# Optimization experiments

Measured on AMD Instinct MI355X. Metric: run time of the kernel, lower is better.

Reference implementation:

```python
import jax, jax.numpy as jnp
import numpy as np

N = 50000      # nodes
E = 800000     # edges
F_IN = 11      # node feature dim (from docstring)
HID = 128      # hidden_channels
NC = 16        # num_classes
G = 64         # number of graphs in the batch
NEG_SLOPE = 0.2


def gat_layer(h_in, src, dst, W, a_src, a_dst, b, n_nodes):
    """Single-head GATConv with self-loops (PyG defaults, edge_attr unused)."""
    h = h_in @ W                                   # [N, C]
    alpha_s = h @ a_src                            # [N]
    alpha_d = h @ a_dst                            # [N]
    e = jax.nn.leaky_relu(alpha_s[src] + alpha_d[dst], NEG_SLOPE)  # [E']
    # segment softmax over incoming edges of each dst node
    m = jax.ops.segment_max(e, dst, num_segments=n_nodes)
    ex = jnp.exp(e - m[dst])
    den = jax.ops.segment_sum(ex, dst, num_segments=n_nodes)
    alpha = ex / den[dst]                          # [E']
    out = jax.ops.segment_sum(alpha[:, None] * h[src], dst, num_segments=n_nodes)
    return out + b


def setup_inputs() -> dict:
    key = jax.random.key(0)
    ks = jax.random.split(key, 16)
    glorot = lambda k, fi, fo: jax.random.normal(k, (fi, fo), jnp.float32) * np.float32(1.0 / np.sqrt(fi))
    inp = {
        "x": jax.random.normal(ks[0], (N, F_IN), jnp.float32),
        "edge_index": jax.random.randint(ks[1], (2, E), 0, N, dtype=jnp.int32),
        "edge_attr": jax.random.normal(ks[2], (E, 17), jnp.float32),
        "batch": jnp.sort(jax.random.randint(ks[3], (N,), 0, G, dtype=jnp.int32)),
        "W1": glorot(ks[4], F_IN, HID), "as1": jax.random.normal(ks[5], (HID,)) * 0.1,
        "ad1": jax.random.normal(ks[6], (HID,)) * 0.1, "b1": jnp.zeros((HID,), jnp.float32),
        "W2": glorot(ks[7], HID, HID), "as2": jax.random.normal(ks[8], (HID,)) * 0.1,
        "ad2": jax.random.normal(ks[9], (HID,)) * 0.1, "b2": jnp.zeros((HID,), jnp.float32),
        "W3": glorot(ks[10], HID, NC), "as3": jax.random.normal(ks[11], (NC,)) * 0.1,
        "ad3": jax.random.normal(ks[12], (NC,)) * 0.1, "b3": jnp.zeros((NC,), jnp.float32),
    }
    return inp


def reference(x, edge_index, edge_attr, batch,
              W1, as1, ad1, b1, W2, as2, ad2, b2, W3, as3, ad3, b3):
    n = x.shape[0]
    loop = jnp.arange(n, dtype=edge_index.dtype)
    src = jnp.concatenate([edge_index[0], loop])   # add self-loops
    dst = jnp.concatenate([edge_index[1], loop])

    h = jax.nn.relu(gat_layer(x, src, dst, W1, as1, ad1, b1, n))
    h = jax.nn.relu(gat_layer(h, src, dst, W2, as2, ad2, b2, n))
    h = jax.nn.relu(gat_layer(h, src, dst, W3, as3, ad3, b3, n))

    # global mean pool over graphs
    sums = jax.ops.segment_sum(h, batch, num_segments=G)              # [G, NC]
    cnts = jax.ops.segment_sum(jnp.ones((n,), h.dtype), batch, num_segments=G)
    pooled = sums / jnp.maximum(cnts, 1.0)[:, None]
    # dropout is identity in eval mode
    return jax.nn.sigmoid(pooled)
```

## Files before the change

kernel.cpp:

```cpp
#include <hip/hip_runtime.h>
#include <hip/hip_bf16.h>
#include <hip/hip_fp16.h>
#include <math.h>

#define N_NODES 50000
#define N_EDGES 800000
#define F_IN    11
#define HID     128
#define NC      16
#define NG      64
#define E_TOT   (N_EDGES + N_NODES)
#define NBLK_POOL ((N_NODES + 255) / 256)
#define NEG_SLOPE 0.2f

#define NB   ((N_NODES + 63) >> 6)
#define BCAP 4096

typedef _Float16 half_t;
typedef __attribute__((ext_vector_type(4))) _Float16 half4;
typedef __attribute__((ext_vector_type(8))) _Float16 half8;
typedef __attribute__((ext_vector_type(4))) float f32x4;

__device__ __forceinline__ float leaky(float x) { return x >= 0.f ? x : NEG_SLOPE * x; }


__global__ void zero_nb_kernel(int* __restrict__ gcount) {
    int i = threadIdx.x;
    if (i < NB) gcount[i] = 0;
}

__global__ __launch_bounds__(256) void bucket_hist_kernel(const int* __restrict__ ei,
                                                          int* __restrict__ gcount) {
    __shared__ int cnt[NB];
    int tid = threadIdx.x;
    for (int i = tid; i < NB; i += 256) cnt[i] = 0;
    __syncthreads();
    int e0 = blockIdx.x * 4096 + tid;
#pragma unroll
    for (int k = 0; k < 16; ++k) {
        int e = e0 + k * 256;
        if (e < N_EDGES) atomicAdd(&cnt[ei[N_EDGES + e] >> 6], 1);
    }
    __syncthreads();
    for (int i = tid; i < NB; i += 256)
        if (cnt[i]) atomicAdd(&gcount[i], cnt[i]);
}

__global__ void scanB_kernel(const int* __restrict__ gcount, int* __restrict__ bOff,
                             int* __restrict__ gcur) {
    __shared__ int ls[1024];
    int tid = threadIdx.x;
    int v = 0;
    if (tid < NB) {
        int sl = N_NODES - (tid << 6);
        sl = sl > 64 ? 64 : sl;
        v = gcount[tid] + sl;
    }
    ls[tid] = v;
    __syncthreads();
    for (int ofs = 1; ofs < 1024; ofs <<= 1) {
        int x = (tid >= ofs) ? ls[tid - ofs] : 0;
        __syncthreads();
        ls[tid] += x;
        __syncthreads();
    }
    int excl = (tid > 0) ? ls[tid - 1] : 0;
    if (tid < NB) { bOff[tid] = excl; gcur[tid] = excl; }
    if (tid == 0) bOff[NB] = E_TOT;
}

__global__ __launch_bounds__(256) void bucket_scatter_kernel(const int* __restrict__ ei,
                                                             int* __restrict__ gcur,
                                                             uint2* __restrict__ pairs) {
    __shared__ int cnt[NB];
    __shared__ int base[NB];
    int tid = threadIdx.x;
    for (int i = tid; i < NB; i += 256) cnt[i] = 0;
    __syncthreads();
    int s[16], d[16];
    int e0 = blockIdx.x * 4096 + tid;
#pragma unroll
    for (int k = 0; k < 16; ++k) {
        int e = e0 + k * 256;
        if (e < N_EDGES) { s[k] = ei[e]; d[k] = ei[N_EDGES + e]; }
        else if (e < E_TOT) { s[k] = d[k] = e - N_EDGES; }
        else d[k] = -1;
        if (d[k] >= 0) atomicAdd(&cnt[d[k] >> 6], 1);
    }
    __syncthreads();
    for (int i = tid; i < NB; i += 256)
        base[i] = cnt[i] ? atomicAdd(&gcur[i], cnt[i]) : 0;
    __syncthreads();
    for (int i = tid; i < NB; i += 256) cnt[i] = 0;
    __syncthreads();
#pragma unroll
    for (int k = 0; k < 16; ++k) {
        if (d[k] >= 0) {
            int b = d[k] >> 6;
            int r = atomicAdd(&cnt[b], 1);
            pairs[base[b] + r] = make_uint2((unsigned)s[k], (unsigned)d[k]);
        }
    }
}

__global__ __launch_bounds__(256) void csr_finalize_kernel(const uint2* __restrict__ pairs,
                                                           const int* __restrict__ bOff,
                                                           int* __restrict__ off,
                                                           int* __restrict__ csr) {
    __shared__ uint2 lp[BCAP];
    __shared__ int deg[64], offs[65], cnt[64];
    int b = blockIdx.x, tid = threadIdx.x;
    int d0 = b << 6;
    int nd = N_NODES - d0; nd = nd > 64 ? 64 : nd;
    int lo = bOff[b], hi = bOff[b + 1], n = hi - lo;
    if (tid < 64) { deg[tid] = 0; cnt[tid] = 0; }
    __syncthreads();
    bool staged = (n <= BCAP);
    for (int i = tid; i < n; i += 256) {
        uint2 p = pairs[lo + i];
        if (staged) lp[i] = p;
        atomicAdd(&deg[(int)p.y - d0], 1);
    }
    __syncthreads();
    if (tid == 0) {
        int a = 0;
#pragma unroll
        for (int i = 0; i < 64; ++i) { offs[i] = a; a += deg[i]; }
        offs[64] = a;
    }
    __syncthreads();
    if (tid < nd) off[d0 + tid] = lo + offs[tid];
    if (b == (int)gridDim.x - 1 && tid == 0) off[N_NODES] = E_TOT;
    for (int i = tid; i < n; i += 256) {
        uint2 p = staged ? lp[i] : pairs[lo + i];
        int ld = (int)p.y - d0;
        int r = atomicAdd(&cnt[ld], 1);
        csr[lo + offs[ld] + r] = (int)p.x;
    }
}


__global__ void prep_w2t_kernel(const float* __restrict__ W2, half_t* __restrict__ W2T) {
    int id = blockIdx.x * 256 + threadIdx.x;
    if (id < HID * HID) {
        int col = id >> 7, k = id & 127;
        W2T[id] = (half_t)W2[k * HID + col];
    }
}


__global__ void gemm1_kernel(const float* __restrict__ x, const float* __restrict__ W,
                             const float* __restrict__ a_s, const float* __restrict__ a_d,
                             half_t* __restrict__ h16,
                             float* __restrict__ asv, float* __restrict__ adv) {
    __shared__ float xr[F_IN];
    __shared__ float red[4];
    int row = blockIdx.x;
    int t = threadIdx.x;
    if (t < F_IN) xr[t] = x[row * F_IN + t];
    __syncthreads();
    float acc = 0.f;
#pragma unroll
    for (int k = 0; k < F_IN; ++k) acc = fmaf(xr[k], W[k * HID + t], acc);
    h16[(size_t)row * HID + t] = (half_t)acc;
    float ps = acc * a_s[t], pd = acc * a_d[t];
#pragma unroll
    for (int m = 32; m; m >>= 1) { ps += __shfl_xor(ps, m); pd += __shfl_xor(pd, m); }
    int lane = t & 63, wid = t >> 6;
    if (lane == 0) { red[wid * 2] = ps; red[wid * 2 + 1] = pd; }
    __syncthreads();
    if (t == 0) { asv[row] = red[0] + red[2]; adv[row] = red[1] + red[3]; }
}


__global__ __launch_bounds__(256) void gemm2_mfma_kernel(
    const half_t* __restrict__ A, const half_t* __restrict__ W2T,
    const float* __restrict__ a_s, const float* __restrict__ a_d,
    half_t* __restrict__ outp, float* __restrict__ asv, float* __restrict__ adv) {
    int wid = threadIdx.x >> 6;
    int lane = threadIdx.x & 63;
    int row0 = blockIdx.x * 64 + wid * 16;
    int rl = lane & 15;
    int kg = lane >> 4;
    int arow = row0 + rl;
    if (arow >= N_NODES) arow = N_NODES - 1;
    const half8* Ap = (const half8*)(A + (size_t)arow * HID);
    half8 afrag[4];
#pragma unroll
    for (int kk = 0; kk < 4; ++kk) afrag[kk] = Ap[kk * 4 + kg];
    float ps[4] = {0.f, 0.f, 0.f, 0.f}, pd[4] = {0.f, 0.f, 0.f, 0.f};
#pragma unroll
    for (int ct = 0; ct < 8; ++ct) {
        f32x4 acc = {0.f, 0.f, 0.f, 0.f};
        const half8* Bp = (const half8*)(W2T + (size_t)(ct * 16 + rl) * HID);
#pragma unroll
        for (int kk = 0; kk < 4; ++kk)
            acc = __builtin_amdgcn_mfma_f32_16x16x32_f16(afrag[kk], Bp[kk * 4 + kg], acc, 0, 0, 0);
        int col = ct * 16 + rl;
        float as_c = a_s[col], ad_c = a_d[col];
#pragma unroll
        for (int i = 0; i < 4; ++i) {
            int r = row0 + kg * 4 + i;
            ps[i] = fmaf(acc[i], as_c, ps[i]);
            pd[i] = fmaf(acc[i], ad_c, pd[i]);
            if (r < N_NODES) outp[(size_t)r * HID + col] = (half_t)acc[i];
        }
    }
#pragma unroll
    for (int m = 1; m <= 8; m <<= 1) {
#pragma unroll
        for (int i = 0; i < 4; ++i) { ps[i] += __shfl_xor(ps[i], m); pd[i] += __shfl_xor(pd[i], m); }
    }
    if (rl == 0) {
#pragma unroll
        for (int i = 0; i < 4; ++i) {
            int r = row0 + kg * 4 + i;
            if (r < N_NODES) { asv[r] = ps[i]; adv[r] = pd[i]; }
        }
    }
}


__global__ __launch_bounds__(256) void gemm3_kernel(const half_t* __restrict__ A16,
                                                    const float* __restrict__ W,
                                                    const float* __restrict__ a_s,
                                                    const float* __restrict__ a_d,
                                                    float* __restrict__ outp,
                                                    float* __restrict__ asv,
                                                    float* __restrict__ adv) {
    __shared__ float hs[16][HID + 1];
    int tid = threadIdx.x;
    int row0 = blockIdx.x * 16;
    for (int i = tid; i < 16 * HID; i += 256) {
        int r = i >> 7, c = i & 127;
        int gr = row0 + r;
        hs[r][c] = (gr < N_NODES) ? (float)A16[(size_t)gr * HID + c] : 0.f;
    }
    __syncthreads();
    int col = tid & 15, r = tid >> 4;
    float acc = 0.f;
#pragma unroll 4
    for (int k = 0; k < HID; ++k) acc = fmaf(hs[r][k], W[k * NC + col], acc);
    int gr = row0 + r;
    float ps = acc * a_s[col], pd = acc * a_d[col];
#pragma unroll
    for (int m = 1; m <= 8; m <<= 1) { ps += __shfl_xor(ps, m); pd += __shfl_xor(pd, m); }
    if (gr < N_NODES) {
        outp[(size_t)gr * NC + col] = acc;
        if (col == 0) { asv[gr] = ps; adv[gr] = pd; }
    }
}


__global__ __launch_bounds__(256) void agg128_kernel(
    const half_t* __restrict__ h16, const int* __restrict__ off, const int* __restrict__ csr,
    const float* __restrict__ asv, const float* __restrict__ adv,
    const float* __restrict__ bias, half_t* __restrict__ outp) {
    int lane = threadIdx.x & 63;
    int n = (blockIdx.x * blockDim.x + threadIdx.x) >> 6;
    if (n >= N_NODES) return;
    int o0 = off[n], o1 = off[n + 1];
    float ad_n = adv[n];
    int half = lane >> 5;
    int qc = lane & 31;
    const half4* hp = (const half4*)h16;
    float m = -INFINITY, den = 0.f;
    float4 acc = make_float4(0.f, 0.f, 0.f, 0.f);
    for (int base = o0; base < o1; base += 64) {
        int j = base + lane;
        bool valid = j < o1;
        int s = valid ? csr[j] : 0;
        float e = valid ? leaky(asv[s] + ad_n) : -INFINITY;
        float cm = e;
#pragma unroll
        for (int k = 32; k; k >>= 1) cm = fmaxf(cm, __shfl_xor(cm, k));
        float nm = fmaxf(m, cm);
        float rs = __expf(m - nm);
        den *= rs; acc.x *= rs; acc.y *= rs; acc.z *= rs; acc.w *= rs;
        float w = valid ? __expf(e - nm) : 0.f;
        float ws = w;
#pragma unroll
        for (int k = 32; k; k >>= 1) ws += __shfl_xor(ws, k);
        den += ws;
        m = nm;
        int cnt = min(64, o1 - base);
        int t = 0;
        for (; t + 8 <= cnt; t += 8) {
            int e0 = t + half, e1 = t + 2 + half, e2 = t + 4 + half, e3 = t + 6 + half;
            int s0 = __shfl(s, e0), s1 = __shfl(s, e1), s2 = __shfl(s, e2), s3 = __shfl(s, e3);
            float w0 = __shfl(w, e0), w1 = __shfl(w, e1), w2 = __shfl(w, e2), w3 = __shfl(w, e3);
            half4 v0 = hp[(size_t)s0 * 32 + qc];
            half4 v1 = hp[(size_t)s1 * 32 + qc];
            half4 v2 = hp[(size_t)s2 * 32 + qc];
            half4 v3 = hp[(size_t)s3 * 32 + qc];
            acc.x = fmaf(w0, (float)v0.x, acc.x); acc.y = fmaf(w0, (float)v0.y, acc.y);
            acc.z = fmaf(w0, (float)v0.z, acc.z); acc.w = fmaf(w0, (float)v0.w, acc.w);
            acc.x = fmaf(w1, (float)v1.x, acc.x); acc.y = fmaf(w1, (float)v1.y, acc.y);
            acc.z = fmaf(w1, (float)v1.z, acc.z); acc.w = fmaf(w1, (float)v1.w, acc.w);
            acc.x = fmaf(w2, (float)v2.x, acc.x); acc.y = fmaf(w2, (float)v2.y, acc.y);
            acc.z = fmaf(w2, (float)v2.z, acc.z); acc.w = fmaf(w2, (float)v2.w, acc.w);
            acc.x = fmaf(w3, (float)v3.x, acc.x); acc.y = fmaf(w3, (float)v3.y, acc.y);
            acc.z = fmaf(w3, (float)v3.z, acc.z); acc.w = fmaf(w3, (float)v3.w, acc.w);
        }
        for (; t + 2 <= cnt; t += 2) {
            int e0 = t + half;
            int s0 = __shfl(s, e0);
            float w0 = __shfl(w, e0);
            half4 v0 = hp[(size_t)s0 * 32 + qc];
            acc.x = fmaf(w0, (float)v0.x, acc.x); acc.y = fmaf(w0, (float)v0.y, acc.y);
            acc.z = fmaf(w0, (float)v0.z, acc.z); acc.w = fmaf(w0, (float)v0.w, acc.w);
        }
        if (t < cnt) {
            int s0 = __shfl(s, t);
            float w0 = __shfl(w, t);
            if (half == 0) {
                half4 v0 = hp[(size_t)s0 * 32 + qc];
                acc.x = fmaf(w0, (float)v0.x, acc.x); acc.y = fmaf(w0, (float)v0.y, acc.y);
                acc.z = fmaf(w0, (float)v0.z, acc.z); acc.w = fmaf(w0, (float)v0.w, acc.w);
            }
        }
    }
    acc.x += __shfl_xor(acc.x, 32); acc.y += __shfl_xor(acc.y, 32);
    acc.z += __shfl_xor(acc.z, 32); acc.w += __shfl_xor(acc.w, 32);
    if (half == 0) {
        float inv = 1.f / den;
        float4 bv = ((const float4*)bias)[qc];
        half4 o;
        o.x = (half_t)fmaxf(fmaf(acc.x, inv, bv.x), 0.f);
        o.y = (half_t)fmaxf(fmaf(acc.y, inv, bv.y), 0.f);
        o.z = (half_t)fmaxf(fmaf(acc.z, inv, bv.z), 0.f);
        o.w = (half_t)fmaxf(fmaf(acc.w, inv, bv.w), 0.f);
        ((half4*)outp)[(size_t)n * 32 + qc] = o;
    }
}

__global__ __launch_bounds__(256) void agg16_kernel(
    const float* __restrict__ h, const int* __restrict__ off, const int* __restrict__ csr,
    const float* __restrict__ asv, const float* __restrict__ adv,
    const float* __restrict__ bias, float* __restrict__ outp) {
    int lane = threadIdx.x & 63;
    int n = (blockIdx.x * blockDim.x + threadIdx.x) >> 6;
    if (n >= N_NODES) return;
    int o0 = off[n], o1 = off[n + 1];
    float ad_n = adv[n];
    int g = lane >> 3, pr = lane & 7;
    const float2* hp = (const float2*)h;
    float m = -INFINITY, den = 0.f;
    float ax = 0.f, ay = 0.f;
    for (int base = o0; base < o1; base += 64) {
        int j = base + lane;
        bool valid = j < o1;
        int s = valid ? csr[j] : 0;
        float e = valid ? leaky(asv[s] + ad_n) : -INFINITY;
        float cm = e;
#pragma unroll
        for (int k = 32; k; k >>= 1) cm = fmaxf(cm, __shfl_xor(cm, k));
        float nm = fmaxf(m, cm);
        float rs = __expf(m - nm);
        den *= rs; ax *= rs; ay *= rs;
        float w = valid ? __expf(e - nm) : 0.f;
        float ws = w;
#pragma unroll
        for (int k = 32; k; k >>= 1) ws += __shfl_xor(ws, k);
        den += ws;
        m = nm;
        int cnt = min(64, o1 - base);
        for (int t = g; t < cnt; t += 8) {
            int st = __shfl(s, t);
            float wt = __shfl(w, t);
            float2 v = hp[(size_t)st * 8 + pr];
            ax = fmaf(wt, v.x, ax); ay = fmaf(wt, v.y, ay);
        }
    }
    ax += __shfl_xor(ax, 8);  ay += __shfl_xor(ay, 8);
    ax += __shfl_xor(ax, 16); ay += __shfl_xor(ay, 16);
    ax += __shfl_xor(ax, 32); ay += __shfl_xor(ay, 32);
    if (g == 0) {
        float inv = 1.f / den;
        float vx = fmaxf(fmaf(ax, inv, bias[pr * 2]), 0.f);
        float vy = fmaxf(fmaf(ay, inv, bias[pr * 2 + 1]), 0.f);
        ((float2*)outp)[(size_t)n * 8 + pr] = make_float2(vx, vy);
    }
}


__global__ void pool_partial_kernel(const float* __restrict__ h3, const int* __restrict__ batch,
                                    float* __restrict__ part) {
    __shared__ float sp[NG * 17];
    int tid = threadIdx.x;
    for (int i = tid; i < NG * 17; i += 256) sp[i] = 0.f;
    __syncthreads();
    int n = blockIdx.x * 256 + tid;
    if (n < N_NODES) {
        int g = batch[n];
        const float4* hv = (const float4*)(h3 + (size_t)n * NC);
#pragma unroll
        for (int j = 0; j < 4; ++j) {
            float4 v = hv[j];
            atomicAdd(&sp[g * 17 + j * 4 + 0], v.x);
            atomicAdd(&sp[g * 17 + j * 4 + 1], v.y);
            atomicAdd(&sp[g * 17 + j * 4 + 2], v.z);
            atomicAdd(&sp[g * 17 + j * 4 + 3], v.w);
        }
        atomicAdd(&sp[g * 17 + 16], 1.f);
    }
    __syncthreads();
    for (int i = tid; i < NG * 17; i += 256) part[(size_t)blockIdx.x * (NG * 17) + i] = sp[i];
}

__global__ void pool_final_kernel(const float* __restrict__ part, float* __restrict__ outp) {
    int tid = threadIdx.x;
    int g = tid >> 4, c = tid & 15;
    float sum = 0.f, cnt = 0.f;
    for (int b = 0; b < NBLK_POOL; ++b) {
        sum += part[(size_t)b * (NG * 17) + g * 17 + c];
        cnt += part[(size_t)b * (NG * 17) + g * 17 + 16];
    }
    float v = sum / fmaxf(cnt, 1.f);
    outp[g * NC + c] = 1.f / (1.f + __expf(-v));
}


extern "C" void kernel_launch(void* const* d_in, const int* in_sizes, int n_in,
                              void* d_out, int out_size, void* d_ws, size_t ws_size,
                              hipStream_t stream) {
    const float* x   = (const float*)d_in[0];
    const int*   ei  = (const int*)d_in[1];
    const int*   bat = (const int*)d_in[3];
    const float* W1  = (const float*)d_in[4];
    const float* as1 = (const float*)d_in[5];
    const float* ad1 = (const float*)d_in[6];
    const float* b1  = (const float*)d_in[7];
    const float* W2  = (const float*)d_in[8];
    const float* as2 = (const float*)d_in[9];
    const float* ad2 = (const float*)d_in[10];
    const float* b2  = (const float*)d_in[11];
    const float* W3  = (const float*)d_in[12];
    const float* as3 = (const float*)d_in[13];
    const float* ad3 = (const float*)d_in[14];
    const float* b3  = (const float*)d_in[15];
    float* outp = (float*)d_out;

    char* p = (char*)d_ws;
    auto carve = [&](size_t bytes) {
        char* r = p;
        p += (bytes + 255) & ~(size_t)255;
        return r;
    };
    int*    off    = (int*)carve((size_t)(N_NODES + 1) * 4);
    int*    csr    = (int*)carve((size_t)E_TOT * 4);
    int*    gcount = (int*)carve((size_t)NB * 4);
    int*    bOff   = (int*)carve((size_t)(NB + 1) * 4);
    int*    gcur   = (int*)carve((size_t)NB * 4);
    uint2*  pairs  = (uint2*)carve((size_t)E_TOT * 8);
    half_t* h16    = (half_t*)carve((size_t)N_NODES * HID * 2);
    half_t* o16    = (half_t*)carve((size_t)N_NODES * HID * 2);
    half_t* W2T    = (half_t*)carve((size_t)HID * HID * 2);
    float*  h3     = (float*)carve((size_t)N_NODES * NC * 4);
    float*  o3     = (float*)carve((size_t)N_NODES * NC * 4);
    float*  asv    = (float*)carve((size_t)N_NODES * 4);
    float*  adv    = (float*)carve((size_t)N_NODES * 4);
    float*  part   = (float*)carve((size_t)NBLK_POOL * NG * 17 * 4);

    zero_nb_kernel<<<1, 1024, 0, stream>>>(gcount);
    bucket_hist_kernel<<<(N_EDGES + 4095) / 4096, 256, 0, stream>>>(ei, gcount);
    scanB_kernel<<<1, 1024, 0, stream>>>(gcount, bOff, gcur);
    bucket_scatter_kernel<<<(E_TOT + 4095) / 4096, 256, 0, stream>>>(ei, gcur, pairs);
    csr_finalize_kernel<<<NB, 256, 0, stream>>>(pairs, bOff, off, csr);

    prep_w2t_kernel<<<(HID * HID + 255) / 256, 256, 0, stream>>>(W2, W2T);

    gemm1_kernel<<<N_NODES, 128, 0, stream>>>(x, W1, as1, ad1, h16, asv, adv);
    agg128_kernel<<<(N_NODES + 3) / 4, 256, 0, stream>>>(h16, off, csr, asv, adv, b1, o16);

    gemm2_mfma_kernel<<<(N_NODES + 63) / 64, 256, 0, stream>>>(o16, W2T, as2, ad2, h16, asv, adv);
    agg128_kernel<<<(N_NODES + 3) / 4, 256, 0, stream>>>(h16, off, csr, asv, adv, b2, o16);

    gemm3_kernel<<<(N_NODES + 15) / 16, 256, 0, stream>>>(o16, W3, as3, ad3, h3, asv, adv);
    agg16_kernel<<<(N_NODES + 3) / 4, 256, 0, stream>>>(h3, off, csr, asv, adv, b3, o3);

    pool_partial_kernel<<<NBLK_POOL, 256, 0, stream>>>(o3, bat, part);
    pool_final_kernel<<<1, 1024, 0, stream>>>(part, outp);
}
```

Baseline: 343.0 us.

## Compact CSR pairs, store layer-3 features in fp16, fuse W2T prep, deepen gather unroll

Source ids and local destination offsets are packed into one 32-bit word, halving the traffic of the bucket pairs buffer. The layer-3 projected features are now stored in fp16, halving gather bytes in agg16. The W2 transpose is folded into the histogram kernel, a memset replaces the zero kernel, and the agg128 inner loop is unrolled to 16 edges so more gathers are in flight. The packing assumes source ids fit in 16 bits, but N is 50000 and fits; fp16 storage adds a little rounding.

```diff
diff --git a/kernel.cpp b/kernel.cpp
--- a/kernel.cpp
+++ b/kernel.cpp
@@ -15,8 +15,10 @@
 
 #define NB   ((N_NODES + 63) >> 6)
 #define BCAP 4096
+#define NHB  ((N_EDGES + 4095) / 4096)
 
 typedef _Float16 half_t;
+typedef __attribute__((ext_vector_type(2))) _Float16 half2v;
 typedef __attribute__((ext_vector_type(4))) _Float16 half4;
 typedef __attribute__((ext_vector_type(8))) _Float16 half8;
 typedef __attribute__((ext_vector_type(4))) float f32x4;
@@ -24,15 +26,20 @@
 __device__ __forceinline__ float leaky(float x) { return x >= 0.f ? x : NEG_SLOPE * x; }
 
 
-__global__ void zero_nb_kernel(int* __restrict__ gcount) {
-    int i = threadIdx.x;
-    if (i < NB) gcount[i] = 0;
-}
-
-__global__ __launch_bounds__(256) void bucket_hist_kernel(const int* __restrict__ ei,
-                                                          int* __restrict__ gcount) {
+__global__ __launch_bounds__(256) void bucket_hist_w2t_kernel(const int* __restrict__ ei,
+                                                              int* __restrict__ gcount,
+                                                              const float* __restrict__ W2,
+                                                              half_t* __restrict__ W2T) {
+    int tid = threadIdx.x;
+    if (blockIdx.x >= NHB) {
+        int id = (blockIdx.x - NHB) * 256 + tid;
+        if (id < HID * HID) {
+            int col = id >> 7, k = id & 127;
+            W2T[id] = (half_t)W2[k * HID + col];
+        }
+        return;
+    }
     __shared__ int cnt[NB];
-    int tid = threadIdx.x;
     for (int i = tid; i < NB; i += 256) cnt[i] = 0;
     __syncthreads();
     int e0 = blockIdx.x * 4096 + tid;
@@ -71,7 +78,7 @@
 
 __global__ __launch_bounds__(256) void bucket_scatter_kernel(const int* __restrict__ ei,
                                                              int* __restrict__ gcur,
-                                                             uint2* __restrict__ pairs) {
+                                                             unsigned* __restrict__ pairs) {
     __shared__ int cnt[NB];
     __shared__ int base[NB];
     int tid = threadIdx.x;
@@ -98,16 +105,16 @@
         if (d[k] >= 0) {
             int b = d[k] >> 6;
             int r = atomicAdd(&cnt[b], 1);
-            pairs[base[b] + r] = make_uint2((unsigned)s[k], (unsigned)d[k]);
-        }
-    }
-}
-
-__global__ __launch_bounds__(256) void csr_finalize_kernel(const uint2* __restrict__ pairs,
+            pairs[base[b] + r] = (unsigned)s[k] | ((unsigned)(d[k] & 63) << 16);
+        }
+    }
+}
+
+__global__ __launch_bounds__(256) void csr_finalize_kernel(const unsigned* __restrict__ pairs,
                                                            const int* __restrict__ bOff,
                                                            int* __restrict__ off,
                                                            int* __restrict__ csr) {
-    __shared__ uint2 lp[BCAP];
+    __shared__ unsigned lp[BCAP];
     __shared__ int deg[64], offs[65], cnt[64];
     int b = blockIdx.x, tid = threadIdx.x;
     int d0 = b << 6;
@@ -117,9 +124,9 @@
     __syncthreads();
     bool staged = (n <= BCAP);
     for (int i = tid; i < n; i += 256) {
-        uint2 p = pairs[lo + i];
+        unsigned p = pairs[lo + i];
         if (staged) lp[i] = p;
-        atomicAdd(&deg[(int)p.y - d0], 1);
+        atomicAdd(&deg[p >> 16], 1);
     }
     __syncthreads();
     if (tid == 0) {
@@ -132,19 +139,10 @@
     if (tid < nd) off[d0 + tid] = lo + offs[tid];
     if (b == (int)gridDim.x - 1 && tid == 0) off[N_NODES] = E_TOT;
     for (int i = tid; i < n; i += 256) {
-        uint2 p = staged ? lp[i] : pairs[lo + i];
-        int ld = (int)p.y - d0;
+        unsigned p = staged ? lp[i] : pairs[lo + i];
+        int ld = p >> 16;
         int r = atomicAdd(&cnt[ld], 1);
-        csr[lo + offs[ld] + r] = (int)p.x;
-    }
-}
-
-
-__global__ void prep_w2t_kernel(const float* __restrict__ W2, half_t* __restrict__ W2T) {
-    int id = blockIdx.x * 256 + threadIdx.x;
-    if (id < HID * HID) {
-        int col = id >> 7, k = id & 127;
-        W2T[id] = (half_t)W2[k * HID + col];
+        csr[lo + offs[ld] + r] = (int)(p & 0xFFFF);
     }
 }
 
@@ -225,7 +223,7 @@
                                                     const float* __restrict__ W,
                                                     const float* __restrict__ a_s,
                                                     const float* __restrict__ a_d,
-                                                    float* __restrict__ outp,
+                                                    half_t* __restrict__ outp,
                                                     float* __restrict__ asv,
                                                     float* __restrict__ adv) {
     __shared__ float hs[16][HID + 1];
@@ -246,7 +244,7 @@
 #pragma unroll
     for (int m = 1; m <= 8; m <<= 1) { ps += __shfl_xor(ps, m); pd += __shfl_xor(pd, m); }
     if (gr < N_NODES) {
-        outp[(size_t)gr * NC + col] = acc;
+        outp[(size_t)gr * NC + col] = (half_t)acc;
         if (col == 0) { asv[gr] = ps; adv[gr] = pd; }
     }
 }
@@ -285,27 +283,43 @@
         m = nm;
         int cnt = min(64, o1 - base);
         int t = 0;
+        for (; t + 16 <= cnt; t += 16) {
+            int sv[8]; float wv[8]; half4 vv[8];
+#pragma unroll
+            for (int u = 0; u < 8; ++u) {
+                sv[u] = __shfl(s, t + 2 * u + half);
+                wv[u] = __shfl(w, t + 2 * u + half);
+            }
+#pragma unroll
+            for (int u = 0; u < 8; ++u) vv[u] = hp[(size_t)sv[u] * 32 + qc];
+#pragma unroll
+            for (int u = 0; u < 8; ++u) {
+                acc.x = fmaf(wv[u], (float)vv[u].x, acc.x);
+                acc.y = fmaf(wv[u], (float)vv[u].y, acc.y);
+                acc.z = fmaf(wv[u], (float)vv[u].z, acc.z);
+                acc.w = fmaf(wv[u], (float)vv[u].w, acc.w);
+            }
+        }
         for (; t + 8 <= cnt; t += 8) {
-            int e0 = t + half, e1 = t + 2 + half, e2 = t + 4 + half, e3 = t + 6 + half;
-            int s0 = __shfl(s, e0), s1 = __shfl(s, e1), s2 = __shfl(s, e2), s3 = __shfl(s, e3);
-            float w0 = __shfl(w, e0), w1 = __shfl(w, e1), w2 = __shfl(w, e2), w3 = __shfl(w, e3);
-            half4 v0 = hp[(size_t)s0 * 32 + qc];
-            half4 v1 = hp[(size_t)s1 * 32 + qc];
-            half4 v2 = hp[(size_t)s2 * 32 + qc];
-            half4 v3 = hp[(size_t)s3 * 32 + qc];
-            acc.x = fmaf(w0, (float)v0.x, acc.x); acc.y = fmaf(w0, (float)v0.y, acc.y);
-            acc.z = fmaf(w0, (float)v0.z, acc.z); acc.w = fmaf(w0, (float)v0.w, acc.w);
-            acc.x = fmaf(w1, (float)v1.x, acc.x); acc.y = fmaf(w1, (float)v1.y, acc.y);
-            acc.z = fmaf(w1, (float)v1.z, acc.z); acc.w = fmaf(w1, (float)v1.w, acc.w);
-            acc.x = fmaf(w2, (float)v2.x, acc.x); acc.y = fmaf(w2, (float)v2.y, acc.y);
-            acc.z = fmaf(w2, (float)v2.z, acc.z); acc.w = fmaf(w2, (float)v2.w, acc.w);
-            acc.x = fmaf(w3, (float)v3.x, acc.x); acc.y = fmaf(w3, (float)v3.y, acc.y);
-            acc.z = fmaf(w3, (float)v3.z, acc.z); acc.w = fmaf(w3, (float)v3.w, acc.w);
+            int sv[4]; float wv[4]; half4 vv[4];
+#pragma unroll
+            for (int u = 0; u < 4; ++u) {
+                sv[u] = __shfl(s, t + 2 * u + half);
+                wv[u] = __shfl(w, t + 2 * u + half);
+            }
+#pragma unroll
+            for (int u = 0; u < 4; ++u) vv[u] = hp[(size_t)sv[u] * 32 + qc];
+#pragma unroll
+            for (int u = 0; u < 4; ++u) {
+                acc.x = fmaf(wv[u], (float)vv[u].x, acc.x);
+                acc.y = fmaf(wv[u], (float)vv[u].y, acc.y);
+                acc.z = fmaf(wv[u], (float)vv[u].z, acc.z);
+                acc.w = fmaf(wv[u], (float)vv[u].w, acc.w);
+            }
         }
         for (; t + 2 <= cnt; t += 2) {
-            int e0 = t + half;
-            int s0 = __shfl(s, e0);
-            float w0 = __shfl(w, e0);
+            int s0 = __shfl(s, t + half);
+            float w0 = __shfl(w, t + half);
             half4 v0 = hp[(size_t)s0 * 32 + qc];
             acc.x = fmaf(w0, (float)v0.x, acc.x); acc.y = fmaf(w0, (float)v0.y, acc.y);
             acc.z = fmaf(w0, (float)v0.z, acc.z); acc.w = fmaf(w0, (float)v0.w, acc.w);
@@ -335,7 +349,7 @@
 }
 
 __global__ __launch_bounds__(256) void agg16_kernel(
-    const float* __restrict__ h, const int* __restrict__ off, const int* __restrict__ csr,
+    const half_t* __restrict__ h, const int* __restrict__ off, const int* __restrict__ csr,
     const float* __restrict__ asv, const float* __restrict__ adv,
     const float* __restrict__ bias, float* __restrict__ outp) {
     int lane = threadIdx.x & 63;
@@ -344,7 +358,7 @@
     int o0 = off[n], o1 = off[n + 1];
     float ad_n = adv[n];
     int g = lane >> 3, pr = lane & 7;
-    const float2* hp = (const float2*)h;
+    const half2v* hp = (const half2v*)h;
     float m = -INFINITY, den = 0.f;
     float ax = 0.f, ay = 0.f;
     for (int base = o0; base < o1; base += 64) {
@@ -368,8 +382,8 @@
         for (int t = g; t < cnt; t += 8) {
             int st = __shfl(s, t);
             float wt = __shfl(w, t);
-            float2 v = hp[(size_t)st * 8 + pr];
-            ax = fmaf(wt, v.x, ax); ay = fmaf(wt, v.y, ay);
+            half2v v = hp[(size_t)st * 8 + pr];
+            ax = fmaf(wt, (float)v.x, ax); ay = fmaf(wt, (float)v.y, ay);
         }
     }
     ax += __shfl_xor(ax, 8);  ay += __shfl_xor(ay, 8);
@@ -447,29 +461,27 @@
         p += (bytes + 255) & ~(size_t)255;
         return r;
     };
-    int*    off    = (int*)carve((size_t)(N_NODES + 1) * 4);
-    int*    csr    = (int*)carve((size_t)E_TOT * 4);
-    int*    gcount = (int*)carve((size_t)NB * 4);
-    int*    bOff   = (int*)carve((size_t)(NB + 1) * 4);
-    int*    gcur   = (int*)carve((size_t)NB * 4);
-    uint2*  pairs  = (uint2*)carve((size_t)E_TOT * 8);
-    half_t* h16    = (half_t*)carve((size_t)N_NODES * HID * 2);
-    half_t* o16    = (half_t*)carve((size_t)N_NODES * HID * 2);
-    half_t* W2T    = (half_t*)carve((size_t)HID * HID * 2);
-    float*  h3     = (float*)carve((size_t)N_NODES * NC * 4);
-    float*  o3     = (float*)carve((size_t)N_NODES * NC * 4);
-    float*  asv    = (float*)carve((size_t)N_NODES * 4);
-    float*  adv    = (float*)carve((size_t)N_NODES * 4);
-    float*  part   = (float*)carve((size_t)NBLK_POOL * NG * 17 * 4);
-
-    zero_nb_kernel<<<1, 1024, 0, stream>>>(gcount);
-    bucket_hist_kernel<<<(N_EDGES + 4095) / 4096, 256, 0, stream>>>(ei, gcount);
+    int*      off    = (int*)carve((size_t)(N_NODES + 1) * 4);
+    int*      csr    = (int*)carve((size_t)E_TOT * 4);
+    int*      gcount = (int*)carve((size_t)NB * 4);
+    int*      bOff   = (int*)carve((size_t)(NB + 1) * 4);
+    int*      gcur   = (int*)carve((size_t)NB * 4);
+    unsigned* pairs  = (unsigned*)carve((size_t)E_TOT * 4);
+    half_t*   h16    = (half_t*)carve((size_t)N_NODES * HID * 2);
+    half_t*   o16    = (half_t*)carve((size_t)N_NODES * HID * 2);
+    half_t*   W2T    = (half_t*)carve((size_t)HID * HID * 2);
+    half_t*   h3     = (half_t*)carve((size_t)N_NODES * NC * 2);
+    float*    o3     = (float*)carve((size_t)N_NODES * NC * 4);
+    float*    asv    = (float*)carve((size_t)N_NODES * 4);
+    float*    adv    = (float*)carve((size_t)N_NODES * 4);
+    float*    part   = (float*)carve((size_t)NBLK_POOL * NG * 17 * 4);
+
+    hipMemsetAsync(gcount, 0, (size_t)NB * 4, stream);
+    bucket_hist_w2t_kernel<<<NHB + 64, 256, 0, stream>>>(ei, gcount, W2, W2T);
     scanB_kernel<<<1, 1024, 0, stream>>>(gcount, bOff, gcur);
     bucket_scatter_kernel<<<(E_TOT + 4095) / 4096, 256, 0, stream>>>(ei, gcur, pairs);
     csr_finalize_kernel<<<NB, 256, 0, stream>>>(pairs, bOff, off, csr);
 
-    prep_w2t_kernel<<<(HID * HID + 255) / 256, 256, 0, stream>>>(W2, W2T);
-
     gemm1_kernel<<<N_NODES, 128, 0, stream>>>(x, W1, as1, ad1, h16, asv, adv);
     agg128_kernel<<<(N_NODES + 3) / 4, 256, 0, stream>>>(h16, off, csr, asv, adv, b1, o16);
 
```

Result: no change. 340.7 us (-0.6%).
